# Optimization experiments

Hardware: AMD Instinct MI355X
Metric: run time of the kernel (lower is better)

The kernel has to match this reference:

```python
import jax, jax.numpy as jnp
import numpy as np

NUM_TRACKS = [128, 256, 512, 1024, 2048, 64, 32, 1024]
B, S, D = 8, 2048, 1536
H = len(NUM_TRACKS)
T = max(NUM_TRACKS)  # num_output_tracks (padded)


def setup_inputs() -> dict:
    key = jax.random.key(0)
    kx, kw, kb, ki = jax.random.split(key, 4)
    x = jax.random.normal(kx, (B, S, D), dtype=jnp.float32)
    # Padded per-species weights: columns >= num_tracks[i] are zero, matching the
    # original's jnp.pad of head logits with zeros.
    track_mask = (jnp.arange(T)[None, :] < jnp.asarray(NUM_TRACKS)[:, None]).astype(jnp.float32)  # [H, T]
    W = jax.random.normal(kw, (H, D, T), dtype=jnp.float32) * 0.02
    W = W * track_mask[:, None, :]
    b = jax.random.normal(kb, (H, T), dtype=jnp.float32) * 0.02
    b = b * track_mask
    head_idx = jax.random.randint(ki, (B,), 0, H, dtype=jnp.int32)
    return {"x": x, "head_idx": head_idx, "W": W, "b": b}


def reference(x, head_idx, W, b):
    # Dense compute of ALL species heads (faithful to original which evaluates
    # every head over the full batch), then per-sample selection via head_idx
    # (equivalent to the original's sequential jnp.where masking).
    logits_all = jnp.einsum('bsd,hdt->bhst', x, W) + b[None, :, None, :]  # [B, H, S, T]
    sel = head_idx[:, None, None, None].astype(jnp.int32)                 # [B, 1, 1, 1]
    logits = jnp.take_along_axis(logits_all, sel, axis=1)[:, 0]           # [B, S, T]
    return logits
```

## Files before the change

kernel.cpp:

```cpp
#include <hip/hip_runtime.h>
#include <hip/hip_bf16.h>
#include <stdint.h>

#define NB 8
#define NS 2048
#define ND 1536
#define NT 2048
#define NH 8
#define NK2 (ND / 64)

__constant__ int c_tiles[NH] = {1, 2, 4, 8, 16, 1, 1, 8};

typedef short bf16x8 __attribute__((ext_vector_type(8)));
typedef unsigned short u16x8 __attribute__((ext_vector_type(8)));
typedef float f32x4 __attribute__((ext_vector_type(4)));

__device__ __forceinline__ unsigned short f2bf(float f) {
    union { float f; unsigned u; } a; a.f = f;
    unsigned r = a.u + 0x7fffu + ((a.u >> 16) & 1u);
    return (unsigned short)(r >> 16);
}

#define XBLK 24576
__global__ void cvt_kernel(const float* __restrict__ x,
                           const float* __restrict__ W,
                           const int* __restrict__ hidx,
                           unsigned short* __restrict__ xb,
                           unsigned short* __restrict__ Wt) {
    const int bid = blockIdx.x;
    const int tid = threadIdx.x;
    if (bid < XBLK) {
        const size_t i = (size_t)bid * 256 + tid;
        float4 v = ((const float4*)x)[i];
        ushort4 o;
        o.x = f2bf(v.x); o.y = f2bf(v.y); o.z = f2bf(v.z); o.w = f2bf(v.w);
        ((ushort4*)xb)[i] = o;
        return;
    }
    const int wid = bid - XBLK;
    const int h = wid / (32 * 24);
    const int rem = wid % (32 * 24);
    const int t0 = (rem % 32) * 64;
    const int d0 = (rem / 32) * 64;
    bool used = false;
    for (int i = 0; i < NB; ++i) used |= (hidx[i] == h);
    if (!used || t0 >= c_tiles[h] * 128) return;

    __shared__ float tile[64][69];
#pragma unroll
    for (int i = 0; i < 4; ++i) {
        const int idx = tid + i * 256;
        const int d = idx >> 4, c = (idx & 15) * 4;
        float4 v = *(const float4*)&W[((size_t)h * ND + d0 + d) * NT + t0 + c];
        tile[d][c] = v.x; tile[d][c + 1] = v.y;
        tile[d][c + 2] = v.z; tile[d][c + 3] = v.w;
    }
    __syncthreads();
    const int t = tid >> 2, dc = (tid & 3) * 16;
    u16x8 o0, o1;
#pragma unroll
    for (int j = 0; j < 8; ++j) o0[j] = f2bf(tile[dc + j][t]);
#pragma unroll
    for (int j = 0; j < 8; ++j) o1[j] = f2bf(tile[dc + 8 + j][t]);
    unsigned short* p = Wt + ((size_t)h * NT + t0 + t) * ND + d0 + dc;
    *(u16x8*)p = o0;
    *(u16x8*)(p + 8) = o1;
}

#define GLDS(g, l)                                                      \
    __builtin_amdgcn_global_load_lds(                                   \
        (const __attribute__((address_space(1))) void*)(g),             \
        (__attribute__((address_space(3))) void*)(l), 16, 0, 0)

__global__ __launch_bounds__(512) void gemm_kernel(
    const unsigned short* __restrict__ xb,
    const unsigned short* __restrict__ wt,
    const float* __restrict__ bias,
    const int* __restrict__ hidx,
    float* __restrict__ out)
{
    const int tid = threadIdx.x;
    const int id = blockIdx.x;

    int hh[NB], tl[NB];
    int P = 0;
#pragma unroll
    for (int b = 0; b < NB; ++b) {
        hh[b] = hidx[b];
        tl[b] = c_tiles[hh[b]];
        P += tl[b];
    }
    const int C = 8 * P;

    int batch, m0, n0;
    if (id >= C) {
        const int Pz = 128 - P;
        const int z = id - C;
        int p = z % Pz;
        const int m = z / Pz;
        int b = 0;
        while (p >= 16 - tl[b]) { p -= 16 - tl[b]; ++b; }
        batch = b; n0 = (tl[b] + p) * 128; m0 = m * 256;
        float* outb = out + (size_t)batch * NS * NT;
        const int row = tid >> 1;
        const int c0 = (tid & 1) * 64;
        float4 zv = make_float4(0.f, 0.f, 0.f, 0.f);
        float4* ptr = (float4*)(outb + (size_t)(m0 + row) * NT + (n0 + c0));
#pragma unroll
        for (int j = 0; j < 16; ++j) ptr[j] = zv;
        return;
    }
    {
        int p = id % P;
        const int m = id / P;
        int b = 0;
        while (p >= tl[b]) { p -= tl[b]; ++b; }
        batch = b; n0 = p * 128; m0 = m * 256;
    }
    const int h = hh[batch];
    float* outb = out + (size_t)batch * NS * NT;

    __shared__ unsigned short As[256 * 64];
    __shared__ unsigned short Bs[128 * 64];

    const int lane = tid & 63;
    const int wave = tid >> 6;
    const int wm = (wave >> 1) * 64;
    const int wn = (wave & 1) * 64;
    const int fr = lane & 15;
    const int q = lane >> 4;

    const unsigned short* ga[4];
    unsigned short* la[4];
#pragma unroll
    for (int j = 0; j < 4; ++j) {
        const int c = tid + 512 * j;
        const int r = c >> 3, gc = (c & 7) ^ (r & 7);
        ga[j] = xb + ((size_t)batch * NS + m0 + r) * ND + gc * 8;
        la[j] = As + c * 8;
    }
    const unsigned short* gb[2];
    unsigned short* lb[2];
#pragma unroll
    for (int j = 0; j < 2; ++j) {
        const int c = tid + 512 * j;
        const int r = c >> 3, gc = (c & 7) ^ (r & 7);
        gb[j] = wt + ((size_t)h * NT + n0 + r) * ND + gc * 8;
        lb[j] = Bs + c * 8;
    }

    const int sw0 = ((q) ^ (fr & 7)) * 8;
    const int sw1 = ((q + 4) ^ (fr & 7)) * 8;

    f32x4 acc[4][4] = {};

    for (int it = 0; it < NK2; ++it) {
#pragma unroll
        for (int j = 0; j < 4; ++j) GLDS(ga[j], la[j]);
#pragma unroll
        for (int j = 0; j < 2; ++j) GLDS(gb[j], lb[j]);
        __syncthreads();
#pragma unroll
        for (int kk = 0; kk < 2; ++kk) {
            const int sw = kk ? sw1 : sw0;
            bf16x8 af[4], bfr[4];
#pragma unroll
            for (int mi = 0; mi < 4; ++mi)
                af[mi] = *(const bf16x8*)(As + (wm + mi * 16 + fr) * 64 + sw);
#pragma unroll
            for (int ni = 0; ni < 4; ++ni)
                bfr[ni] = *(const bf16x8*)(Bs + (wn + ni * 16 + fr) * 64 + sw);
#pragma unroll
            for (int mi = 0; mi < 4; ++mi)
#pragma unroll
                for (int ni = 0; ni < 4; ++ni)
                    acc[mi][ni] = __builtin_amdgcn_mfma_f32_16x16x32_bf16(
                        af[mi], bfr[ni], acc[mi][ni], 0, 0, 0);
        }
        __syncthreads();
#pragma unroll
        for (int j = 0; j < 4; ++j) ga[j] += 64;
#pragma unroll
        for (int j = 0; j < 2; ++j) gb[j] += 64;
    }

    float bv[4];
#pragma unroll
    for (int ni = 0; ni < 4; ++ni)
        bv[ni] = bias[(size_t)h * NT + n0 + wn + ni * 16 + fr];

    const int rbase = m0 + wm + q * 4;
#pragma unroll
    for (int mi = 0; mi < 4; ++mi) {
#pragma unroll
        for (int r = 0; r < 4; ++r) {
            float* op = outb + (size_t)(rbase + mi * 16 + r) * NT + n0 + wn + fr;
#pragma unroll
            for (int ni = 0; ni < 4; ++ni)
                op[ni * 16] = acc[mi][ni][r] + bv[ni];
        }
    }
}

extern "C" void kernel_launch(void* const* d_in, const int* in_sizes, int n_in,
                              void* d_out, int out_size, void* d_ws, size_t ws_size,
                              hipStream_t stream) {
    const float* x    = (const float*)d_in[0];
    const int*   hidx = (const int*)d_in[1];
    const float* W    = (const float*)d_in[2];
    const float* bias = (const float*)d_in[3];
    float* out = (float*)d_out;

    unsigned short* xb = (unsigned short*)d_ws;
    unsigned short* wt = xb + (size_t)NB * NS * ND;

    cvt_kernel<<<dim3(XBLK + 32 * 24 * NH), dim3(256), 0, stream>>>(
        x, W, hidx, xb, wt);
    gemm_kernel<<<dim3(1024), dim3(512), 0, stream>>>(xb, wt, bias, hidx, out);
}
```

Measured before the change: 322.6 us.

## Double-buffer LDS tiles with K-step 32 to overlap loads and MFMA

Splits the GEMM K loop into 32-wide steps and uses two LDS buffers for A and B. The next tile is prefetched with global_load_lds while the current one is consumed, and only one barrier is left per iteration. The aim is to hide global-to-LDS latency behind the MFMA work. The cost is twice as many iterations and barriers, plus a narrower 4-way XOR swizzle on 64-byte rows that may raise LDS bank conflicts.

```diff
diff --git a/kernel.cpp b/kernel.cpp
--- a/kernel.cpp
+++ b/kernel.cpp
@@ -7,7 +7,7 @@
 #define ND 1536
 #define NT 2048
 #define NH 8
-#define NK2 (ND / 64)
+#define NK1 (ND / 32)
 
 __constant__ int c_tiles[NH] = {1, 2, 4, 8, 16, 1, 1, 8};
 
@@ -120,8 +120,8 @@
     const int h = hh[batch];
     float* outb = out + (size_t)batch * NS * NT;
 
-    __shared__ unsigned short As[256 * 64];
-    __shared__ unsigned short Bs[128 * 64];
+    __shared__ unsigned short As[2][256 * 32];
+    __shared__ unsigned short Bs[2][128 * 32];
 
     const int lane = tid & 63;
     const int wave = tid >> 6;
@@ -130,58 +130,56 @@
     const int fr = lane & 15;
     const int q = lane >> 4;
 
-    const unsigned short* ga[4];
-    unsigned short* la[4];
-#pragma unroll
-    for (int j = 0; j < 4; ++j) {
-        const int c = tid + 512 * j;
-        const int r = c >> 3, gc = (c & 7) ^ (r & 7);
-        ga[j] = xb + ((size_t)batch * NS + m0 + r) * ND + gc * 8;
-        la[j] = As + c * 8;
-    }
-    const unsigned short* gb[2];
-    unsigned short* lb[2];
+    const unsigned short* ga[2];
+    int laoff[2];
 #pragma unroll
     for (int j = 0; j < 2; ++j) {
         const int c = tid + 512 * j;
-        const int r = c >> 3, gc = (c & 7) ^ (r & 7);
-        gb[j] = wt + ((size_t)h * NT + n0 + r) * ND + gc * 8;
-        lb[j] = Bs + c * 8;
-    }
-
-    const int sw0 = ((q) ^ (fr & 7)) * 8;
-    const int sw1 = ((q + 4) ^ (fr & 7)) * 8;
+        const int r = c >> 2, gc = (c & 3) ^ (r & 3);
+        ga[j] = xb + ((size_t)batch * NS + m0 + r) * ND + gc * 8;
+        laoff[j] = c * 8;
+    }
+    const unsigned short* gb;
+    int lboff;
+    {
+        const int c = tid;
+        const int r = c >> 2, gc = (c & 3) ^ (r & 3);
+        gb = wt + ((size_t)h * NT + n0 + r) * ND + gc * 8;
+        lboff = c * 8;
+    }
+
+    const int sw = (q ^ (fr & 3)) * 8;
 
     f32x4 acc[4][4] = {};
 
-    for (int it = 0; it < NK2; ++it) {
-#pragma unroll
-        for (int j = 0; j < 4; ++j) GLDS(ga[j], la[j]);
-#pragma unroll
-        for (int j = 0; j < 2; ++j) GLDS(gb[j], lb[j]);
+    GLDS(ga[0], &As[0][laoff[0]]);
+    GLDS(ga[1], &As[0][laoff[1]]);
+    GLDS(gb, &Bs[0][lboff]);
+    ga[0] += 32; ga[1] += 32; gb += 32;
+
+    for (int it = 0; it < NK1; ++it) {
+        const int cur = it & 1;
         __syncthreads();
-#pragma unroll
-        for (int kk = 0; kk < 2; ++kk) {
-            const int sw = kk ? sw1 : sw0;
-            bf16x8 af[4], bfr[4];
-#pragma unroll
-            for (int mi = 0; mi < 4; ++mi)
-                af[mi] = *(const bf16x8*)(As + (wm + mi * 16 + fr) * 64 + sw);
+        if (it + 1 < NK1) {
+            const int nxt = cur ^ 1;
+            GLDS(ga[0], &As[nxt][laoff[0]]);
+            GLDS(ga[1], &As[nxt][laoff[1]]);
+            GLDS(gb, &Bs[nxt][lboff]);
+            ga[0] += 32; ga[1] += 32; gb += 32;
+        }
+        bf16x8 af[4], bfr[4];
+#pragma unroll
+        for (int mi = 0; mi < 4; ++mi)
+            af[mi] = *(const bf16x8*)(&As[cur][(wm + mi * 16 + fr) * 32 + sw]);
+#pragma unroll
+        for (int ni = 0; ni < 4; ++ni)
+            bfr[ni] = *(const bf16x8*)(&Bs[cur][(wn + ni * 16 + fr) * 32 + sw]);
+#pragma unroll
+        for (int mi = 0; mi < 4; ++mi)
 #pragma unroll
             for (int ni = 0; ni < 4; ++ni)
-                bfr[ni] = *(const bf16x8*)(Bs + (wn + ni * 16 + fr) * 64 + sw);
-#pragma unroll
-            for (int mi = 0; mi < 4; ++mi)
-#pragma unroll
-                for (int ni = 0; ni < 4; ++ni)
-                    acc[mi][ni] = __builtin_amdgcn_mfma_f32_16x16x32_bf16(
-                        af[mi], bfr[ni], acc[mi][ni], 0, 0, 0);
-        }
-        __syncthreads();
-#pragma unroll
-        for (int j = 0; j < 4; ++j) ga[j] += 64;
-#pragma unroll
-        for (int j = 0; j < 2; ++j) gb[j] += 64;
+                acc[mi][ni] = __builtin_amdgcn_mfma_f32_16x16x32_bf16(
+                    af[mi], bfr[ni], acc[mi][ni], 0, 0, 0);
     }
 
     float bv[4];
```

Measured after the change: 332.1 us. 3.0% more time.
